# Kernel tuning notes

Measured on AMD Instinct MI355X. Metric: run time of the kernel, lower is better.

The kernel has to match this reference:

```python
import jax, jax.numpy as jnp
import numpy as np

NUM_CLASSES = 80
TOPK = 9
EPS_OVERLAPS = 1e-6  # mmdet BboxOverlaps2D: union clamped to eps
EPS_YOLOV6 = 1e-9    # yolov6_iou_calculator: eps added to union


def _pairwise_iou(b1, b2, eps, add_eps):
    # b1: (..., M, 4), b2: (..., N, 4) xyxy -> (..., M, N)
    lt = jnp.maximum(b1[..., :, None, :2], b2[..., None, :, :2])
    rb = jnp.minimum(b1[..., :, None, 2:], b2[..., None, :, 2:])
    wh = jnp.clip(rb - lt, 0.0)
    overlap = wh[..., 0] * wh[..., 1]
    a1 = (b1[..., 2] - b1[..., 0]) * (b1[..., 3] - b1[..., 1])
    a2 = (b2[..., 2] - b2[..., 0]) * (b2[..., 3] - b2[..., 1])
    union = a1[..., :, None] + a2[..., None, :] - overlap
    return overlap / (union + eps) if add_eps else overlap / jnp.maximum(union, eps)


def _assign(pred_bboxes, priors, gt_labels, gt_bboxes, pad_bbox_flag, num_level_priors):
    num_level_priors = tuple(int(n) for n in np.asarray(num_level_priors))
    # priors (x, y, stride_w, stride_h) -> 5*stride cell boxes in xyxy
    cell_half = priors[:, 2:] * 2.5
    prior_boxes = jnp.concatenate([priors[:, :2] - cell_half, priors[:, :2] + cell_half], axis=-1)
    bs, num_gt = gt_bboxes.shape[0], gt_bboxes.shape[1]
    num_priors = priors.shape[0]
    gt_flat = gt_bboxes.reshape(-1, 4)

    # step 1: IoU between all priors and all gts
    overlaps = _pairwise_iou(gt_flat, prior_boxes, EPS_OVERLAPS, False).reshape(bs, num_gt, num_priors)

    # step 2: center distances
    gt_cxy = (gt_flat[:, :2] + gt_flat[:, 2:]) * 0.5
    prior_cxy = (prior_boxes[:, :2] + prior_boxes[:, 2:]) * 0.5
    dist = jnp.sqrt(jnp.sum((gt_cxy[:, None, :] - prior_cxy[None, :, :]) ** 2, axis=-1))
    dist = dist.reshape(bs, num_gt, num_priors)

    # step 3: per-level topk closest candidates
    pad_bool = pad_bbox_flag[..., 0] > 0  # (bs, num_gt)
    b_ix = jnp.arange(bs)[:, None, None]
    g_ix = jnp.arange(num_gt)[None, :, None]
    is_in_list, cand_list = [], []
    start = 0
    for pl in num_level_priors:
        k = min(TOPK, pl)
        d_l = jax.lax.dynamic_slice_in_dim(dist, start, pl, axis=-1)
        _, idx = jax.lax.top_k(-d_l, k)  # (bs, num_gt, k) smallest distances
        cand_list.append(idx + start)
        idx_m = jnp.where(pad_bool[..., None], idx, 0)
        counts = jnp.zeros((bs, num_gt, pl), dist.dtype).at[b_ix, g_ix, idx_m].add(1.0)
        is_in_list.append(jnp.where(counts > 1, jnp.zeros_like(counts), counts))
        start += pl
    is_in_candidate = jnp.concatenate(is_in_list, axis=-1)   # (bs, num_gt, num_priors)
    candidate_idxs = jnp.concatenate(cand_list, axis=-1)     # (bs, num_gt, k*levels)

    # step 4: mean + std of candidate IoUs as threshold
    candidate_overlaps = jnp.where(is_in_candidate > 0, overlaps, jnp.zeros_like(overlaps))
    gathered = jnp.take_along_axis(candidate_overlaps, candidate_idxs, axis=-1)
    thr = jnp.mean(gathered, axis=-1, keepdims=True) + jnp.std(gathered, axis=-1, keepdims=True, ddof=1)

    # step 5: keep candidates above threshold
    is_pos = jnp.where(candidate_overlaps > thr, is_in_candidate, jnp.zeros_like(is_in_candidate))

    # step 6: center of prior must lie inside gt box
    lt = prior_cxy[None, None, :, :] - gt_bboxes[:, :, None, :2]
    rb = gt_bboxes[:, :, None, 2:] - prior_cxy[None, None, :, :]
    is_in_gts = (jnp.minimum(lt, rb).min(axis=-1) > 1e-9).astype(gt_bboxes.dtype)

    pos_mask = is_pos * is_in_gts * pad_bbox_flag  # pad flag broadcasts (bs,num_gt,1)

    # resolve priors assigned to multiple gts: keep highest IoU gt
    fg = pos_mask.sum(axis=-2)  # (bs, num_priors)
    best_gt = jnp.argmax(overlaps, axis=1)  # (bs, num_priors)
    is_max = jax.nn.one_hot(best_gt, num_gt, dtype=pos_mask.dtype).transpose(0, 2, 1)
    pos_mask = jnp.where(fg[:, None, :] > 1, is_max, pos_mask)
    fg_mask = pos_mask.sum(axis=-2)                 # (bs, num_priors)
    gt_idx = jnp.argmax(pos_mask, axis=-2)          # (bs, num_priors)

    # targets
    flat_idx = gt_idx + jnp.arange(bs)[:, None] * num_gt
    assigned_labels = gt_labels.reshape(-1)[flat_idx]
    assigned_labels = jnp.where(fg_mask > 0, assigned_labels, NUM_CLASSES)
    assigned_bboxes = gt_bboxes.reshape(-1, 4)[flat_idx]
    assigned_scores = jax.nn.one_hot(assigned_labels, NUM_CLASSES + 1, dtype=gt_bboxes.dtype)[..., :NUM_CLASSES]

    # weight scores by IoU with predictions
    ious = _pairwise_iou(gt_bboxes, pred_bboxes, EPS_YOLOV6, True) * pos_mask
    assigned_scores = assigned_scores * jnp.max(ious, axis=-2)[..., None]
    return assigned_labels, assigned_bboxes, assigned_scores, fg_mask > 0


def setup_inputs() -> dict:
    key = jax.random.key(0)
    k0, k1, k2, k3, k4 = jax.random.split(key, 5)
    bs, num_gt, img = 32, 64, 640
    strides = (8, 16, 32)
    pri = []
    for s in strides:
        n = img // s
        xs = (np.arange(n, dtype=np.float32) + 0.5) * s
        gy, gx = np.meshgrid(xs, xs, indexing='ij')
        pts = np.stack([gx.ravel(), gy.ravel()], axis=1)
        st = np.full((pts.shape[0], 2), s, dtype=np.float32)
        pri.append(np.concatenate([pts, st], axis=1))
    priors = jnp.asarray(np.concatenate(pri, axis=0))  # (8400, 4)
    num_level_priors = (6400, 1600, 400)
    num_priors = priors.shape[0]
    cxy = jax.random.uniform(k0, (bs, num_gt, 2), minval=50.0, maxval=590.0)
    wh = jax.random.uniform(k1, (bs, num_gt, 2), minval=20.0, maxval=200.0)
    gt_bboxes = jnp.concatenate([cxy - wh * 0.5, cxy + wh * 0.5], axis=-1)
    gt_labels = jax.random.randint(k2, (bs, num_gt, 1), 0, NUM_CLASSES)
    pad_bbox_flag = jnp.ones((bs, num_gt, 1), jnp.float32)
    pcxy = priors[None, :, :2] + jax.random.normal(k3, (bs, num_priors, 2)) * 4.0
    pwh = jax.random.uniform(k4, (bs, num_priors, 2), minval=10.0, maxval=150.0)
    pred_bboxes = jnp.concatenate([pcxy - pwh * 0.5, pcxy + pwh * 0.5], axis=-1)
    return {'pred_bboxes': pred_bboxes, 'priors': priors, 'gt_labels': gt_labels,
            'gt_bboxes': gt_bboxes, 'pad_bbox_flag': pad_bbox_flag,
            'num_level_priors': num_level_priors}


def reference(pred_bboxes, priors, gt_labels, gt_bboxes, pad_bbox_flag, num_level_priors):
    return _assign(pred_bboxes, priors, gt_labels, gt_bboxes, pad_bbox_flag, num_level_priors)
```

## Files before the change

kernel.cpp:

```cpp
#include <hip/hip_runtime.h>

#define BS 32
#define NG 64
#define NP 8400
#define NTOPK 9
#define NUM_CLASSES 80
#define NCAND 27

#define TILE 128
#define NTILE 66

__device__ __forceinline__ unsigned long long wave_min_u64_32(unsigned long long k) {
    #pragma unroll
    for (int off = 1; off < 32; off <<= 1) {
        unsigned long long o = __shfl_xor(k, off, 64);
        k = (o < k) ? o : k;
    }
    return k;
}

__global__ __launch_bounds__(256) void k_candidates(
    const float4* __restrict__ gt_bboxes,
    const float*  __restrict__ pad_flag,
    unsigned int* __restrict__ cand)
{
    const int bg   = (blockIdx.x * 256 + threadIdx.x) >> 6;
    const int lane = threadIdx.x & 63;

    const float4 gt  = gt_bboxes[bg];
    const float  pad = pad_flag[bg];
    const float  gcx = (gt.x + gt.z) * 0.5f;
    const float  gcy = (gt.y + gt.w) * 0.5f;
    const float  garea = (gt.z - gt.x) * (gt.w - gt.y);

    const float lvl_s[3] = {8.0f, 16.0f, 32.0f};
    const int   lvl_n[3] = {80, 40, 20};
    const int   lvl_b[3] = {0, 6400, 8000};

    float ov[NCAND];
    int   ixs[NCAND];
    float sum = 0.0f;

    const int dy5 = lane / 5;
    const int dx5 = lane - dy5 * 5;

    #pragma unroll
    for (int L = 0; L < 3; ++L) {
        const float s    = lvl_s[L];
        const int   n    = lvl_n[L];
        const int   base = lvl_b[L];

        int wx = (int)floorf(gcx / s) - 2;
        int wy = (int)floorf(gcy / s) - 2;
        wx = min(max(wx, 0), n - 5);
        wy = min(max(wy, 0), n - 5);

        unsigned long long key = ~0ull;
        if (lane < 25) {
            const int   iy  = wy + dy5;
            const int   ix  = wx + dx5;
            const float py  = ((float)iy + 0.5f) * s;
            const float px  = ((float)ix + 0.5f) * s;
            const float ddx = gcx - px;
            const float ddy = gcy - py;
            const float d   = sqrtf(ddx * ddx + ddy * ddy);
            key = ((unsigned long long)__float_as_uint(d) << 32) |
                  (unsigned int)(base + iy * n + ix);
        }

        const float hx = s * 2.5f;
        #pragma unroll
        for (int q = 0; q < NTOPK; ++q) {
            const unsigned long long m = wave_min_u64_32(key);
            if (key == m) key = ~0ull;

            const int slot = L * NTOPK + q;
            const int idx  = (int)(m & 0xffffffffu);
            const int rel  = idx - base;
            const int iy   = rel / n;
            const int ix   = rel - iy * n;
            const float px = ((float)ix + 0.5f) * s;
            const float py = ((float)iy + 0.5f) * s;
            const float px0 = px - hx, py0 = py - hx;
            const float px1 = px + hx, py1 = py + hx;
            float lx = fmaxf(gt.x, px0), ly = fmaxf(gt.y, py0);
            float rx = fminf(gt.z, px1), ry = fminf(gt.w, py1);
            float w = fmaxf(rx - lx, 0.0f), h = fmaxf(ry - ly, 0.0f);
            float ovl = w * h;
            float parea = (px1 - px0) * (py1 - py0);
            float o = ovl / fmaxf(garea + parea - ovl, 1e-6f);
            ov[slot]  = o;
            ixs[slot] = idx;
            sum += o;
        }
    }

    const float mean = sum / (float)NCAND;
    float var = 0.0f;
    #pragma unroll
    for (int i = 0; i < NCAND; ++i) {
        float d = ov[i] - mean;
        var += d * d;
    }
    const float thr = mean + sqrtf(var / (float)(NCAND - 1));

    unsigned int myval = 0xFFFFFFFFu;
    if (pad > 0.0f) {
        #pragma unroll
        for (int i = 0; i < NCAND; ++i) {
            bool pass = false;
            if (ov[i] > thr) {
                const int   L    = i / NTOPK;
                const float s    = lvl_s[L];
                const int   n    = lvl_n[L];
                const int   base = lvl_b[L];
                const int idx = ixs[i];
                const int rel = idx - base;
                const int iy  = rel / n;
                const int ix  = rel - iy * n;
                const float px = ((float)ix + 0.5f) * s;
                const float py = ((float)iy + 0.5f) * s;
                float mm = fminf(fminf(px - gt.x, py - gt.y),
                                 fminf(gt.z - px, gt.w - py));
                pass = (mm > 1e-9f);
            }
            if (lane == i && pass) myval = (unsigned int)ixs[i];
        }
    }
    if (lane < NCAND) cand[(size_t)bg * NCAND + lane] = myval;
}

__global__ __launch_bounds__(256) void k_write(
    const float4* __restrict__ priors,
    const float4* __restrict__ gt_bboxes,
    const int*    __restrict__ gt_labels,
    const float4* __restrict__ pred_bboxes,
    const unsigned int* __restrict__ cand,
    float* __restrict__ out)
{
    __shared__ float4 s_gt[NG];
    __shared__ int    s_lab[NG];
    __shared__ unsigned long long s_pos[TILE];
    __shared__ int    s_plab[TILE];
    __shared__ float  s_piou[TILE];

    const int b   = blockIdx.y;
    const int tid = threadIdx.x;
    const int p0  = blockIdx.x * TILE;
    const int npr = min(TILE, NP - p0);

    if (tid < NG) {
        s_gt[tid]  = gt_bboxes[b * NG + tid];
        s_lab[tid] = gt_labels[b * NG + tid];
    }
    if (tid < TILE) s_pos[tid] = 0;
    __syncthreads();

    {
        const int g    = tid >> 2;
        const int part = tid & 3;
        if (part < 3) {
            const float s    = (part == 0) ? 8.0f : (part == 1) ? 16.0f : 32.0f;
            const int   n    = (part == 0) ? 80   : (part == 1) ? 40    : 20;
            const int   base = (part == 0) ? 0    : (part == 1) ? 6400  : 8000;
            const float4 gt  = s_gt[g];
            const float  gcx = (gt.x + gt.z) * 0.5f;
            const float  gcy = (gt.y + gt.w) * 0.5f;
            int wx = min(max((int)floorf(gcx / s) - 2, 0), n - 5);
            int wy = min(max((int)floorf(gcy / s) - 2, 0), n - 5);
            const int minidx = base + wy * n + wx;
            const int maxidx = base + (wy + 4) * n + wx + 4;
            if (maxidx >= p0 && minidx < p0 + npr) {
                const unsigned int* e =
                    cand + ((size_t)(b * NG + g)) * NCAND + part * NTOPK;
                #pragma unroll
                for (int k = 0; k < NTOPK; ++k) {
                    unsigned int rel = e[k] - (unsigned int)p0;
                    if (rel < (unsigned int)npr)
                        atomicOr(&s_pos[rel], 1ull << g);
                }
            }
        }
    }
    __syncthreads();

    if (tid < npr) {
        const int p = p0 + tid;
        const size_t bp = (size_t)b * NP + p;
        unsigned long long mask = s_pos[tid];
        int fg = __popcll(mask);
        int gidx = 0;

        if (fg > 1) {
            float4 pr = priors[p];
            float hx = pr.z * 2.5f, hy = pr.w * 2.5f;
            float px0 = pr.x - hx, py0 = pr.y - hy, px1 = pr.x + hx, py1 = pr.y + hy;
            float parea = (px1 - px0) * (py1 - py0);
            float best = -1.0f;
            for (int gg = 0; gg < NG; ++gg) {
                float4 gtb = s_gt[gg];
                float lx = fmaxf(gtb.x, px0), ly = fmaxf(gtb.y, py0);
                float rx = fminf(gtb.z, px1), ry = fminf(gtb.w, py1);
                float w = fmaxf(rx - lx, 0.0f), h = fmaxf(ry - ly, 0.0f);
                float ovl = w * h;
                float ga = (gtb.z - gtb.x) * (gtb.w - gtb.y);
                float v = ovl / fmaxf(ga + parea - ovl, 1e-6f);
                if (v > best) { best = v; gidx = gg; }
            }
        } else if (fg == 1) {
            gidx = __ffsll((unsigned long long)mask) - 1;
        }

        const bool   fgm = fg > 0;
        const float4 gtb = s_gt[gidx];
        const int  label = fgm ? s_lab[gidx] : NUM_CLASSES;
        float iou_w = 0.0f;

        if (fgm) {
            float4 pb = pred_bboxes[bp];
            float lx = fmaxf(gtb.x, pb.x), ly = fmaxf(gtb.y, pb.y);
            float rx = fminf(gtb.z, pb.z), ry = fminf(gtb.w, pb.w);
            float w = fmaxf(rx - lx, 0.0f), h = fmaxf(ry - ly, 0.0f);
            float ov = w * h;
            float ga = (gtb.z - gtb.x) * (gtb.w - gtb.y);
            float pa = (pb.z - pb.x) * (pb.w - pb.y);
            iou_w = ov / (ga + pa - ov + 1e-9f);
        }

        out[bp] = (float)label;
        ((float4*)(out + (size_t)BS * NP))[bp] = gtb;
        out[(size_t)BS * NP * 85 + bp] = fgm ? 1.0f : 0.0f;

        s_plab[tid] = label;
        s_piou[tid] = iou_w;
    }
    __syncthreads();

    const int nfl4 = npr * 20;
    float4* o4 = (float4*)(out + (size_t)BS * NP * 5 + ((size_t)b * NP + p0) * 80);
    for (int q = tid; q < nfl4; q += 256) {
        int pl   = q / 20;
        int comp = q - pl * 20;
        int lab  = s_plab[pl];
        float iw = s_piou[pl];
        int dd = lab - comp * 4;
        float4 v;
        v.x = (dd == 0) ? iw : 0.0f;
        v.y = (dd == 1) ? iw : 0.0f;
        v.z = (dd == 2) ? iw : 0.0f;
        v.w = (dd == 3) ? iw : 0.0f;
        o4[q] = v;
    }
}

extern "C" void kernel_launch(void* const* d_in, const int* in_sizes, int n_in,
                              void* d_out, int out_size, void* d_ws, size_t ws_size,
                              hipStream_t stream) {
    const float4* pred_bboxes = (const float4*)d_in[0];
    const float4* priors      = (const float4*)d_in[1];
    const int*    gt_labels   = (const int*)d_in[2];
    const float4* gt_bboxes   = (const float4*)d_in[3];
    const float*  pad_flag    = (const float*)d_in[4];

    unsigned int* cand = (unsigned int*)d_ws;

    k_candidates<<<dim3(BS * NG * 64 / 256), dim3(256), 0, stream>>>(
        gt_bboxes, pad_flag, cand);

    k_write<<<dim3(NTILE, BS), dim3(256), 0, stream>>>(
        priors, gt_bboxes, gt_labels, pred_bboxes, cand, (float*)d_out);
}
```

Measured before the change: 130.9 us.

## Parallelize candidate levels across waves and double write-kernel tile size

The candidate kernel now gives each GT box a 192-thread block, with one wave per pyramid level, instead of one wave looping serially over all three levels. The 27 IoUs go through shared memory, and 27 threads compute the mean/std threshold and filter in parallel, replacing per-lane register arrays. This shortens the serial shuffle-reduction chain and cuts register pressure. Separately, the write kernel's tile grows from 128 to 256 priors per block, so each block uses all 256 threads and there are half as many blocks doing the per-block GT/candidate setup.

```diff
diff --git a/kernel.cpp b/kernel.cpp
--- a/kernel.cpp
+++ b/kernel.cpp
@@ -7,8 +7,8 @@
 #define NUM_CLASSES 80
 #define NCAND 27
 
-#define TILE 128
-#define NTILE 66
+#define TILE 256
+#define NTILE 33
 
 __device__ __forceinline__ unsigned long long wave_min_u64_32(unsigned long long k) {
     #pragma unroll
@@ -19,13 +19,18 @@
     return k;
 }
 
-__global__ __launch_bounds__(256) void k_candidates(
+__global__ __launch_bounds__(192) void k_candidates(
     const float4* __restrict__ gt_bboxes,
     const float*  __restrict__ pad_flag,
     unsigned int* __restrict__ cand)
 {
-    const int bg   = (blockIdx.x * 256 + threadIdx.x) >> 6;
-    const int lane = threadIdx.x & 63;
+    __shared__ float s_ov[NCAND];
+    __shared__ int   s_ix[NCAND];
+
+    const int bg   = blockIdx.x;
+    const int tid  = threadIdx.x;
+    const int lane = tid & 63;
+    const int L    = tid >> 6;
 
     const float4 gt  = gt_bboxes[bg];
     const float  pad = pad_flag[bg];
@@ -33,101 +38,85 @@
     const float  gcy = (gt.y + gt.w) * 0.5f;
     const float  garea = (gt.z - gt.x) * (gt.w - gt.y);
 
-    const float lvl_s[3] = {8.0f, 16.0f, 32.0f};
-    const int   lvl_n[3] = {80, 40, 20};
-    const int   lvl_b[3] = {0, 6400, 8000};
-
-    float ov[NCAND];
-    int   ixs[NCAND];
-    float sum = 0.0f;
+    const float s    = (L == 0) ? 8.0f : (L == 1) ? 16.0f : 32.0f;
+    const int   n    = (L == 0) ? 80   : (L == 1) ? 40    : 20;
+    const int   base = (L == 0) ? 0    : (L == 1) ? 6400  : 8000;
+
+    int wx = min(max((int)floorf(gcx / s) - 2, 0), n - 5);
+    int wy = min(max((int)floorf(gcy / s) - 2, 0), n - 5);
 
     const int dy5 = lane / 5;
     const int dx5 = lane - dy5 * 5;
-
+    unsigned long long key = ~0ull;
+    if (lane < 25) {
+        const int   iy  = wy + dy5;
+        const int   ix  = wx + dx5;
+        const float py  = ((float)iy + 0.5f) * s;
+        const float px  = ((float)ix + 0.5f) * s;
+        const float ddx = gcx - px;
+        const float ddy = gcy - py;
+        const float d   = sqrtf(ddx * ddx + ddy * ddy);
+        key = ((unsigned long long)__float_as_uint(d) << 32) |
+              (unsigned int)(base + iy * n + ix);
+    }
+
+    const float hx = s * 2.5f;
     #pragma unroll
-    for (int L = 0; L < 3; ++L) {
-        const float s    = lvl_s[L];
-        const int   n    = lvl_n[L];
-        const int   base = lvl_b[L];
-
-        int wx = (int)floorf(gcx / s) - 2;
-        int wy = (int)floorf(gcy / s) - 2;
-        wx = min(max(wx, 0), n - 5);
-        wy = min(max(wy, 0), n - 5);
-
-        unsigned long long key = ~0ull;
-        if (lane < 25) {
-            const int   iy  = wy + dy5;
-            const int   ix  = wx + dx5;
-            const float py  = ((float)iy + 0.5f) * s;
-            const float px  = ((float)ix + 0.5f) * s;
-            const float ddx = gcx - px;
-            const float ddy = gcy - py;
-            const float d   = sqrtf(ddx * ddx + ddy * ddy);
-            key = ((unsigned long long)__float_as_uint(d) << 32) |
-                  (unsigned int)(base + iy * n + ix);
-        }
-
-        const float hx = s * 2.5f;
-        #pragma unroll
-        for (int q = 0; q < NTOPK; ++q) {
-            const unsigned long long m = wave_min_u64_32(key);
-            if (key == m) key = ~0ull;
-
-            const int slot = L * NTOPK + q;
-            const int idx  = (int)(m & 0xffffffffu);
-            const int rel  = idx - base;
-            const int iy   = rel / n;
-            const int ix   = rel - iy * n;
-            const float px = ((float)ix + 0.5f) * s;
-            const float py = ((float)iy + 0.5f) * s;
-            const float px0 = px - hx, py0 = py - hx;
-            const float px1 = px + hx, py1 = py + hx;
-            float lx = fmaxf(gt.x, px0), ly = fmaxf(gt.y, py0);
-            float rx = fminf(gt.z, px1), ry = fminf(gt.w, py1);
-            float w = fmaxf(rx - lx, 0.0f), h = fmaxf(ry - ly, 0.0f);
-            float ovl = w * h;
-            float parea = (px1 - px0) * (py1 - py0);
-            float o = ovl / fmaxf(garea + parea - ovl, 1e-6f);
-            ov[slot]  = o;
-            ixs[slot] = idx;
-            sum += o;
-        }
-    }
-
-    const float mean = sum / (float)NCAND;
-    float var = 0.0f;
-    #pragma unroll
-    for (int i = 0; i < NCAND; ++i) {
-        float d = ov[i] - mean;
-        var += d * d;
-    }
-    const float thr = mean + sqrtf(var / (float)(NCAND - 1));
-
-    unsigned int myval = 0xFFFFFFFFu;
-    if (pad > 0.0f) {
-        #pragma unroll
+    for (int q = 0; q < NTOPK; ++q) {
+        const unsigned long long m = wave_min_u64_32(key);
+        if (key == m) key = ~0ull;
+
+        const int idx  = (int)(m & 0xffffffffu);
+        const int rel  = idx - base;
+        const int iy   = rel / n;
+        const int ix   = rel - iy * n;
+        const float px = ((float)ix + 0.5f) * s;
+        const float py = ((float)iy + 0.5f) * s;
+        const float px0 = px - hx, py0 = py - hx;
+        const float px1 = px + hx, py1 = py + hx;
+        float lx = fmaxf(gt.x, px0), ly = fmaxf(gt.y, py0);
+        float rx = fminf(gt.z, px1), ry = fminf(gt.w, py1);
+        float w = fmaxf(rx - lx, 0.0f), h = fmaxf(ry - ly, 0.0f);
+        float ovl = w * h;
+        float parea = (px1 - px0) * (py1 - py0);
+        float o = ovl / fmaxf(garea + parea - ovl, 1e-6f);
+
+        if (lane == 0) {
+            s_ov[L * NTOPK + q] = o;
+            s_ix[L * NTOPK + q] = idx;
+        }
+    }
+    __syncthreads();
+
+    if (tid < NCAND) {
+        float sum = 0.0f;
+        for (int i = 0; i < NCAND; ++i) sum += s_ov[i];
+        const float mean = sum / (float)NCAND;
+        float var = 0.0f;
         for (int i = 0; i < NCAND; ++i) {
-            bool pass = false;
-            if (ov[i] > thr) {
-                const int   L    = i / NTOPK;
-                const float s    = lvl_s[L];
-                const int   n    = lvl_n[L];
-                const int   base = lvl_b[L];
-                const int idx = ixs[i];
-                const int rel = idx - base;
-                const int iy  = rel / n;
-                const int ix  = rel - iy * n;
-                const float px = ((float)ix + 0.5f) * s;
-                const float py = ((float)iy + 0.5f) * s;
-                float mm = fminf(fminf(px - gt.x, py - gt.y),
-                                 fminf(gt.z - px, gt.w - py));
-                pass = (mm > 1e-9f);
-            }
-            if (lane == i && pass) myval = (unsigned int)ixs[i];
-        }
-    }
-    if (lane < NCAND) cand[(size_t)bg * NCAND + lane] = myval;
+            float d = s_ov[i] - mean;
+            var += d * d;
+        }
+        const float thr = mean + sqrtf(var / (float)(NCAND - 1));
+
+        const int i = tid;
+        unsigned int myval = 0xFFFFFFFFu;
+        if (pad > 0.0f && s_ov[i] > thr) {
+            const float si = (i < 9) ? 8.0f : (i < 18) ? 16.0f : 32.0f;
+            const int   ni = (i < 9) ? 80   : (i < 18) ? 40    : 20;
+            const int   bi = (i < 9) ? 0    : (i < 18) ? 6400  : 8000;
+            const int idx = s_ix[i];
+            const int rel = idx - bi;
+            const int iy  = rel / ni;
+            const int ix  = rel - iy * ni;
+            const float px = ((float)ix + 0.5f) * si;
+            const float py = ((float)iy + 0.5f) * si;
+            float mm = fminf(fminf(px - gt.x, py - gt.y),
+                             fminf(gt.z - px, gt.w - py));
+            if (mm > 1e-9f) myval = (unsigned int)idx;
+        }
+        cand[(size_t)bg * NCAND + i] = myval;
+    }
 }
 
 __global__ __launch_bounds__(256) void k_write(
@@ -153,7 +142,7 @@
         s_gt[tid]  = gt_bboxes[b * NG + tid];
         s_lab[tid] = gt_labels[b * NG + tid];
     }
-    if (tid < TILE) s_pos[tid] = 0;
+    s_pos[tid] = 0;
     __syncthreads();
 
     {
@@ -184,8 +173,11 @@
     }
     __syncthreads();
 
-    if (tid < npr) {
-        const int p = p0 + tid;
+    const int p = p0 + tid;
+    int   label  = NUM_CLASSES;
+    float iou_w  = 0.0f;
+
+    if (p < NP) {
         const size_t bp = (size_t)b * NP + p;
         unsigned long long mask = s_pos[tid];
         int fg = __popcll(mask);
@@ -213,8 +205,7 @@
 
         const bool   fgm = fg > 0;
         const float4 gtb = s_gt[gidx];
-        const int  label = fgm ? s_lab[gidx] : NUM_CLASSES;
-        float iou_w = 0.0f;
+        label = fgm ? s_lab[gidx] : NUM_CLASSES;
 
         if (fgm) {
             float4 pb = pred_bboxes[bp];
@@ -230,10 +221,10 @@
         out[bp] = (float)label;
         ((float4*)(out + (size_t)BS * NP))[bp] = gtb;
         out[(size_t)BS * NP * 85 + bp] = fgm ? 1.0f : 0.0f;
-
-        s_plab[tid] = label;
-        s_piou[tid] = iou_w;
-    }
+    }
+
+    s_plab[tid] = label;
+    s_piou[tid] = iou_w;
     __syncthreads();
 
     const int nfl4 = npr * 20;
@@ -264,7 +255,7 @@
 
     unsigned int* cand = (unsigned int*)d_ws;
 
-    k_candidates<<<dim3(BS * NG * 64 / 256), dim3(256), 0, stream>>>(
+    k_candidates<<<dim3(BS * NG), dim3(192), 0, stream>>>(
         gt_bboxes, pad_flag, cand);
 
     k_write<<<dim3(NTILE, BS), dim3(256), 0, stream>>>(
```

Result: faster. 127.2 us (-2.8%).
